# Optimization experiments

Measured on AMD Instinct MI355X. Metric: run time of the kernel, lower is better.

Reference implementation:

```python
import jax, jax.numpy as jnp
import numpy as np

TEMPERATURE = 0.5
EPS = 1e-8  # torch.nn.CosineSimilarity default eps


def setup_inputs() -> dict:
    key = jax.random.key(0)
    k1, k2 = jax.random.split(key)
    B, D = 4096, 256
    z1 = jax.random.normal(k1, (B, D), dtype=jnp.float32)
    # z2 = perturbed view of z1 so positive cosine sims are positive
    # (original torch code takes log of the RAW cosine sim, which is NaN
    #  for negative positives; realistic SimCLR positives are correlated views)
    z2 = z1 + 0.1 * jax.random.normal(k2, (B, D), dtype=jnp.float32)
    return {"z1": z1, "z2": z2}


def reference(z1, z2):
    B = z1.shape[0]
    z = jnp.concatenate([z1, z2], axis=0)                      # [2B, D]
    norm = jnp.maximum(jnp.linalg.norm(z, axis=-1, keepdims=True), EPS)
    zn = z / norm
    sim = zn @ zn.T                                            # [2B, 2B] cosine sims
    # positives: sim[i, i+B] and sim[i+B, i] (RAW cosine, per original code)
    pos = jnp.concatenate([jnp.diagonal(sim, offset=B),
                           jnp.diagonal(sim, offset=-B)])      # [2B]
    # mask self-similarity diagonal to -inf before exp-sum
    diag = jnp.eye(2 * B, dtype=bool)
    sim_masked = jnp.where(diag, -jnp.inf, sim)
    denom = jnp.sum(jnp.exp(sim_masked / TEMPERATURE), axis=-1)  # [2B]
    loss = -jnp.mean(jnp.log(pos / denom))
    return loss
```

## Files before the change

kernel.cpp:

```cpp
#include <hip/hip_runtime.h>
#include <hip/hip_bf16.h>


#define NROWS 8192
#define BHALF 4096
#define DDIM  256

typedef __attribute__((ext_vector_type(4))) int   i32x4;
typedef __attribute__((ext_vector_type(8))) int   i32x8;
typedef __attribute__((ext_vector_type(4))) float f32x4;

#define SCALE1 0x7F7F7F7F
#define TWO_LOG2E 2.8853900817779268f

__device__ __forceinline__ void load_lds16(const unsigned char* g, unsigned char* l) {
    __builtin_amdgcn_global_load_lds(
        (const __attribute__((address_space(1))) void*)g,
        (__attribute__((address_space(3))) void*)l, 16, 0, 0);
}

__global__ __launch_bounds__(256) void prep_kernel(const float* __restrict__ z1,
                                                   const float* __restrict__ z2,
                                                   unsigned char* __restrict__ zn8,
                                                   float* __restrict__ posPart,
                                                   float* __restrict__ out) {
    __shared__ float sp[4];
    int wave = threadIdx.x >> 6;
    int lane = threadIdx.x & 63;
    int i    = blockIdx.x * 4 + wave;
    float4 a = reinterpret_cast<const float4*>(z1 + (size_t)i * DDIM)[lane];
    float4 b = reinterpret_cast<const float4*>(z2 + (size_t)i * DDIM)[lane];
    float ss1 = a.x * a.x + a.y * a.y + a.z * a.z + a.w * a.w;
    float ss2 = b.x * b.x + b.y * b.y + b.z * b.z + b.w * b.w;
    float dd  = a.x * b.x + a.y * b.y + a.z * b.z + a.w * b.w;
    #pragma unroll
    for (int off = 32; off; off >>= 1) {
        ss1 += __shfl_xor(ss1, off);
        ss2 += __shfl_xor(ss2, off);
        dd  += __shfl_xor(dd, off);
    }
    float n1 = fmaxf(sqrtf(ss1), 1e-8f);
    float n2 = fmaxf(sqrtf(ss2), 1e-8f);
    float i1 = 1.0f / n1, i2 = 1.0f / n2;
    int pa = __builtin_amdgcn_cvt_pk_fp8_f32(a.x * i1, a.y * i1, 0, 0);
    pa     = __builtin_amdgcn_cvt_pk_fp8_f32(a.z * i1, a.w * i1, pa, 1);
    int pb = __builtin_amdgcn_cvt_pk_fp8_f32(b.x * i2, b.y * i2, 0, 0);
    pb     = __builtin_amdgcn_cvt_pk_fp8_f32(b.z * i2, b.w * i2, pb, 1);
    reinterpret_cast<int*>(zn8 + (size_t)i * DDIM)[lane] = pa;
    reinterpret_cast<int*>(zn8 + (size_t)(i + BHALF) * DDIM)[lane] = pb;
    if (lane == 0) sp[wave] = __logf(dd * i1 * i2);
    if (blockIdx.x == 0 && threadIdx.x == 64) out[0] = 0.0f;
    __syncthreads();
    if (threadIdx.x == 0)
        posPart[blockIdx.x] = sp[0] + sp[1] + sp[2] + sp[3];
}

__global__ __launch_bounds__(256, 3) void denom_kernel(const unsigned char* __restrict__ zn8,
                                                       float* __restrict__ P) {
    __shared__ __align__(16) unsigned char sMem[32 * 1024];
    unsigned char* buf0 = sMem;
    unsigned char* buf1 = sMem + 16384;

    int x = blockIdx.x, y = blockIdx.y;
    int bi, bj;
    if (x > y) { bi = y;      bj = x - 1;  }
    else       { bi = 63 - y; bj = 63 - x; }
    int iBase = bi * 128;
    int jBase = bj * 128;
    bool isDiag = (bi == bj);

    int t    = threadIdx.x;
    int lane = t & 63;
    int wave = t >> 6;
    int col  = lane & 15;
    int quad = lane >> 4;
    int wm = wave >> 1, wn = wave & 1;

    int rowL  = t >> 4;
    int chunk = (t & 15) ^ rowL;

    {
        const unsigned char* gA = zn8 + (size_t)(iBase + rowL) * DDIM + chunk * 16;
        #pragma unroll
        for (int q = 0; q < 4; q++)
            load_lds16(gA + q * 4096, buf0 + t * 16 + q * 4096);
        #pragma unroll
        for (int q = 0; q < 4; q++)
            load_lds16(gA + 16384 + q * 4096, buf1 + t * 16 + q * 4096);
    }
    __syncthreads();

    i32x8 af[4][2];
    {
        const unsigned char* aRow = (wm ? buf1 : buf0) + (size_t)col * DDIM;
        #pragma unroll
        for (int mt = 0; mt < 4; mt++)
            #pragma unroll
            for (int ks = 0; ks < 2; ks++) {
                int g0 = ks * 8 + quad * 2;
                i32x4 lo = *(const i32x4*)(aRow + mt * 16 * DDIM + ((g0    ) ^ col) * 16);
                i32x4 hi = *(const i32x4*)(aRow + mt * 16 * DDIM + ((g0 + 1) ^ col) * 16);
                af[mt][ks] = __builtin_shufflevector(lo, hi, 0, 1, 2, 3, 4, 5, 6, 7);
            }
    }
    __syncthreads();

    {
        const unsigned char* gB = zn8 + (size_t)(jBase + rowL) * DDIM + chunk * 16;
        #pragma unroll
        for (int q = 0; q < 4; q++)
            load_lds16(gB + q * 4096, buf0 + t * 16 + q * 4096);
        #pragma unroll
        for (int q = 0; q < 4; q++)
            load_lds16(gB + 16384 + q * 4096, buf1 + t * 16 + q * 4096);
    }
    __syncthreads();

    float rs[4][4];
    #pragma unroll
    for (int mt = 0; mt < 4; mt++)
        #pragma unroll
        for (int r = 0; r < 4; r++) rs[mt][r] = 0.f;

    #pragma unroll
    for (int h = 0; h < 2; h++) {
        const unsigned char* bRow =
            (h ? buf1 : buf0) + (size_t)(wn * 32 + col) * DDIM;

        #pragma unroll
        for (int nt = 0; nt < 2; nt++) {
            i32x8 bfr[2];
            #pragma unroll
            for (int ks = 0; ks < 2; ks++) {
                int g0 = ks * 8 + quad * 2;
                i32x4 lo = *(const i32x4*)(bRow + nt * 16 * DDIM + ((g0    ) ^ col) * 16);
                i32x4 hi = *(const i32x4*)(bRow + nt * 16 * DDIM + ((g0 + 1) ^ col) * 16);
                bfr[ks] = __builtin_shufflevector(lo, hi, 0, 1, 2, 3, 4, 5, 6, 7);
            }

            float csn = 0.f;
            #pragma unroll
            for (int mt = 0; mt < 4; mt++) {
                int gi = iBase + wm * 64 + mt * 16;
                f32x4 acc = {0.f, 0.f, 0.f, 0.f};
                acc = __builtin_amdgcn_mfma_scale_f32_16x16x128_f8f6f4(
                          af[mt][0], bfr[0], acc, 0, 0, 0, SCALE1, 0, SCALE1);
                acc = __builtin_amdgcn_mfma_scale_f32_16x16x128_f8f6f4(
                          af[mt][1], bfr[1], acc, 0, 0, 0, SCALE1, 0, SCALE1);
                bool dtile = (gi == jBase + h * 64 + wn * 32 + nt * 16);
                #pragma unroll
                for (int r = 0; r < 4; r++) {
                    float e = exp2f(acc[r] * TWO_LOG2E);
                    if (dtile && (quad * 4 + r) == col) e = 0.f;
                    rs[mt][r] += e;
                    csn       += e;
                }
            }

            if (!isDiag) {
                csn += __shfl_xor(csn, 16);
                csn += __shfl_xor(csn, 32);
                if (quad == 0)
                    P[(((size_t)bj * 64 + bi) * 2 + wm) * 128
                      + h * 64 + wn * 32 + nt * 16 + col] = csn;
            }
        }
    }

    #pragma unroll
    for (int mt = 0; mt < 4; mt++)
        #pragma unroll
        for (int r = 0; r < 4; r++) {
            float v = rs[mt][r];
            v += __shfl_xor(v, 1);
            v += __shfl_xor(v, 2);
            v += __shfl_xor(v, 4);
            v += __shfl_xor(v, 8);
            rs[mt][r] = v;
        }
    if (col == 0) {
        float* Pr = P + (((size_t)bi * 64 + bj) * 2 + wn) * 128;
        #pragma unroll
        for (int mt = 0; mt < 4; mt++) {
            f32x4 v4 = { rs[mt][0], rs[mt][1], rs[mt][2], rs[mt][3] };
            *reinterpret_cast<f32x4*>(Pr + wm * 64 + mt * 16 + quad * 4) = v4;
        }
    }
}

__global__ __launch_bounds__(256) void loss_kernel(const float* __restrict__ posPart,
                                                   const float* __restrict__ P,
                                                   float* __restrict__ out) {
    __shared__ float sdata[4];
    int t = threadIdx.x;
    int i = blockIdx.x * 256 + t;
    int bi = i >> 7, r = i & 127;
    const float* p = P + ((size_t)bi << 14) + r;
    float d0 = 0.f, d1 = 0.f, d2 = 0.f, d3 = 0.f;
    #pragma unroll
    for (int k = 0; k < 128; k += 4) {
        d0 += p[(k + 0) << 7];
        d1 += p[(k + 1) << 7];
        d2 += p[(k + 2) << 7];
        d3 += p[(k + 3) << 7];
    }
    float s = __logf((d0 + d1) + (d2 + d3));
    if (t < 32) s -= 2.0f * posPart[blockIdx.x * 32 + t];
    #pragma unroll
    for (int off = 32; off; off >>= 1) s += __shfl_xor(s, off);
    if ((t & 63) == 0) sdata[t >> 6] = s;
    __syncthreads();
    if (t == 0)
        atomicAdd(out, (sdata[0] + sdata[1] + sdata[2] + sdata[3]) * (1.0f / NROWS));
}

extern "C" void kernel_launch(void* const* d_in, const int* in_sizes, int n_in,
                              void* d_out, int out_size, void* d_ws, size_t ws_size,
                              hipStream_t stream) {
    const float* z1 = (const float*)d_in[0];
    const float* z2 = (const float*)d_in[1];

    unsigned char* zn8 = (unsigned char*)d_ws;
    float* P       = (float*)((char*)d_ws + (size_t)NROWS * DDIM);
    float* posPart = P + (size_t)64 * 64 * 2 * 128;

    prep_kernel<<<BHALF / 4, 256, 0, stream>>>(z1, z2, zn8, posPart, (float*)d_out);
    denom_kernel<<<dim3(65, 32), 256, 0, stream>>>(zn8, P);
    loss_kernel<<<NROWS / 256, 256, 0, stream>>>(posPart, P, (float*)d_out);
}
```

Measured before the change: 86.65 us.

## Fuse prep, denom and loss kernels into one persistent kernel with grid barriers

```diff
diff --git a/kernel.cpp b/kernel.cpp
--- a/kernel.cpp
+++ b/kernel.cpp
@@ -5,6 +5,7 @@
 #define NROWS 8192
 #define BHALF 4096
 #define DDIM  256
+#define NBLK  768
 
 typedef __attribute__((ext_vector_type(4))) int   i32x4;
 typedef __attribute__((ext_vector_type(8))) int   i32x8;
@@ -19,199 +20,216 @@
         (__attribute__((address_space(3))) void*)l, 16, 0, 0);
 }
 
-__global__ __launch_bounds__(256) void prep_kernel(const float* __restrict__ z1,
-                                                   const float* __restrict__ z2,
-                                                   unsigned char* __restrict__ zn8,
-                                                   float* __restrict__ posPart,
-                                                   float* __restrict__ out) {
-    __shared__ float sp[4];
-    int wave = threadIdx.x >> 6;
-    int lane = threadIdx.x & 63;
-    int i    = blockIdx.x * 4 + wave;
-    float4 a = reinterpret_cast<const float4*>(z1 + (size_t)i * DDIM)[lane];
-    float4 b = reinterpret_cast<const float4*>(z2 + (size_t)i * DDIM)[lane];
-    float ss1 = a.x * a.x + a.y * a.y + a.z * a.z + a.w * a.w;
-    float ss2 = b.x * b.x + b.y * b.y + b.z * b.z + b.w * b.w;
-    float dd  = a.x * b.x + a.y * b.y + a.z * b.z + a.w * b.w;
-    #pragma unroll
-    for (int off = 32; off; off >>= 1) {
-        ss1 += __shfl_xor(ss1, off);
-        ss2 += __shfl_xor(ss2, off);
-        dd  += __shfl_xor(dd, off);
-    }
-    float n1 = fmaxf(sqrtf(ss1), 1e-8f);
-    float n2 = fmaxf(sqrtf(ss2), 1e-8f);
-    float i1 = 1.0f / n1, i2 = 1.0f / n2;
-    int pa = __builtin_amdgcn_cvt_pk_fp8_f32(a.x * i1, a.y * i1, 0, 0);
-    pa     = __builtin_amdgcn_cvt_pk_fp8_f32(a.z * i1, a.w * i1, pa, 1);
-    int pb = __builtin_amdgcn_cvt_pk_fp8_f32(b.x * i2, b.y * i2, 0, 0);
-    pb     = __builtin_amdgcn_cvt_pk_fp8_f32(b.z * i2, b.w * i2, pb, 1);
-    reinterpret_cast<int*>(zn8 + (size_t)i * DDIM)[lane] = pa;
-    reinterpret_cast<int*>(zn8 + (size_t)(i + BHALF) * DDIM)[lane] = pb;
-    if (lane == 0) sp[wave] = __logf(dd * i1 * i2);
-    if (blockIdx.x == 0 && threadIdx.x == 64) out[0] = 0.0f;
+__device__ __forceinline__ void grid_barrier(int* cnt) {
     __syncthreads();
-    if (threadIdx.x == 0)
-        posPart[blockIdx.x] = sp[0] + sp[1] + sp[2] + sp[3];
-}
-
-__global__ __launch_bounds__(256, 3) void denom_kernel(const unsigned char* __restrict__ zn8,
-                                                       float* __restrict__ P) {
+    if (threadIdx.x == 0) {
+        __threadfence();
+        atomicAdd(cnt, 1);
+        while (__hip_atomic_load(cnt, __ATOMIC_RELAXED,
+                                 __HIP_MEMORY_SCOPE_AGENT) < NBLK)
+            __builtin_amdgcn_s_sleep(2);
+        __threadfence();
+    }
+    __syncthreads();
+}
+
+__global__ __launch_bounds__(256, 3) void fused_kernel(
+        const float* __restrict__ z1, const float* __restrict__ z2,
+        unsigned char* __restrict__ zn8, float* __restrict__ posPart,
+        float* __restrict__ P, float* __restrict__ out, int* __restrict__ bar)
+{
     __shared__ __align__(16) unsigned char sMem[32 * 1024];
-    unsigned char* buf0 = sMem;
-    unsigned char* buf1 = sMem + 16384;
-
-    int x = blockIdx.x, y = blockIdx.y;
-    int bi, bj;
-    if (x > y) { bi = y;      bj = x - 1;  }
-    else       { bi = 63 - y; bj = 63 - x; }
-    int iBase = bi * 128;
-    int jBase = bj * 128;
-    bool isDiag = (bi == bj);
-
+    int bid  = blockIdx.x;
     int t    = threadIdx.x;
+    int wave = t >> 6;
     int lane = t & 63;
-    int wave = t >> 6;
-    int col  = lane & 15;
-    int quad = lane >> 4;
-    int wm = wave >> 1, wn = wave & 1;
-
-    int rowL  = t >> 4;
-    int chunk = (t & 15) ^ rowL;
 
     {
-        const unsigned char* gA = zn8 + (size_t)(iBase + rowL) * DDIM + chunk * 16;
+        float* sp = (float*)sMem;
+        for (int vb = bid; vb < 1024; vb += NBLK) {
+            int i = vb * 4 + wave;
+            float4 a = reinterpret_cast<const float4*>(z1 + (size_t)i * DDIM)[lane];
+            float4 b = reinterpret_cast<const float4*>(z2 + (size_t)i * DDIM)[lane];
+            float ss1 = a.x * a.x + a.y * a.y + a.z * a.z + a.w * a.w;
+            float ss2 = b.x * b.x + b.y * b.y + b.z * b.z + b.w * b.w;
+            float dd  = a.x * b.x + a.y * b.y + a.z * b.z + a.w * b.w;
+            #pragma unroll
+            for (int off = 32; off; off >>= 1) {
+                ss1 += __shfl_xor(ss1, off);
+                ss2 += __shfl_xor(ss2, off);
+                dd  += __shfl_xor(dd, off);
+            }
+            float n1 = fmaxf(sqrtf(ss1), 1e-8f);
+            float n2 = fmaxf(sqrtf(ss2), 1e-8f);
+            float i1 = 1.0f / n1, i2 = 1.0f / n2;
+            int pa = __builtin_amdgcn_cvt_pk_fp8_f32(a.x * i1, a.y * i1, 0, 0);
+            pa     = __builtin_amdgcn_cvt_pk_fp8_f32(a.z * i1, a.w * i1, pa, 1);
+            int pb = __builtin_amdgcn_cvt_pk_fp8_f32(b.x * i2, b.y * i2, 0, 0);
+            pb     = __builtin_amdgcn_cvt_pk_fp8_f32(b.z * i2, b.w * i2, pb, 1);
+            reinterpret_cast<int*>(zn8 + (size_t)i * DDIM)[lane] = pa;
+            reinterpret_cast<int*>(zn8 + (size_t)(i + BHALF) * DDIM)[lane] = pb;
+            if (lane == 0) sp[wave] = __logf(dd * i1 * i2);
+            __syncthreads();
+            if (t == 0) posPart[vb] = sp[0] + sp[1] + sp[2] + sp[3];
+            __syncthreads();
+        }
+        if (bid == 0 && t == 0) out[0] = 0.0f;
+    }
+    grid_barrier(bar + 0);
+
+    {
+        unsigned char* buf0 = sMem;
+        unsigned char* buf1 = sMem + 16384;
+        int col  = lane & 15;
+        int quad = lane >> 4;
+        int wm = wave >> 1, wn = wave & 1;
+        int rowL  = t >> 4;
+        int chunk = (t & 15) ^ rowL;
+
+        for (int tile = bid; tile < 2080; tile += NBLK) {
+            __syncthreads();
+
+            int x = tile % 65, y = tile / 65;
+            int bi, bj;
+            if (x > y) { bi = y;      bj = x - 1;  }
+            else       { bi = 63 - y; bj = 63 - x; }
+            int iBase = bi * 128;
+            int jBase = bj * 128;
+            bool isDiag = (bi == bj);
+
+            {
+                const unsigned char* gA = zn8 + (size_t)(iBase + rowL) * DDIM + chunk * 16;
+                #pragma unroll
+                for (int q = 0; q < 4; q++)
+                    load_lds16(gA + q * 4096, buf0 + t * 16 + q * 4096);
+                #pragma unroll
+                for (int q = 0; q < 4; q++)
+                    load_lds16(gA + 16384 + q * 4096, buf1 + t * 16 + q * 4096);
+            }
+            __syncthreads();
+
+            i32x8 af[4][2];
+            {
+                const unsigned char* aRow = (wm ? buf1 : buf0) + (size_t)col * DDIM;
+                #pragma unroll
+                for (int mt = 0; mt < 4; mt++)
+                    #pragma unroll
+                    for (int ks = 0; ks < 2; ks++) {
+                        int g0 = ks * 8 + quad * 2;
+                        i32x4 lo = *(const i32x4*)(aRow + mt * 16 * DDIM + ((g0    ) ^ col) * 16);
+                        i32x4 hi = *(const i32x4*)(aRow + mt * 16 * DDIM + ((g0 + 1) ^ col) * 16);
+                        af[mt][ks] = __builtin_shufflevector(lo, hi, 0, 1, 2, 3, 4, 5, 6, 7);
+                    }
+            }
+            __syncthreads();
+
+            {
+                const unsigned char* gB = zn8 + (size_t)(jBase + rowL) * DDIM + chunk * 16;
+                #pragma unroll
+                for (int q = 0; q < 4; q++)
+                    load_lds16(gB + q * 4096, buf0 + t * 16 + q * 4096);
+                #pragma unroll
+                for (int q = 0; q < 4; q++)
+                    load_lds16(gB + 16384 + q * 4096, buf1 + t * 16 + q * 4096);
+            }
+            __syncthreads();
+
+            float rs[4][4];
+            #pragma unroll
+            for (int mt = 0; mt < 4; mt++)
+                #pragma unroll
+                for (int r = 0; r < 4; r++) rs[mt][r] = 0.f;
+
+            #pragma unroll
+            for (int h = 0; h < 2; h++) {
+                const unsigned char* bRow =
+                    (h ? buf1 : buf0) + (size_t)(wn * 32 + col) * DDIM;
+
+                #pragma unroll
+                for (int nt = 0; nt < 2; nt++) {
+                    i32x8 bfr[2];
+                    #pragma unroll
+                    for (int ks = 0; ks < 2; ks++) {
+                        int g0 = ks * 8 + quad * 2;
+                        i32x4 lo = *(const i32x4*)(bRow + nt * 16 * DDIM + ((g0    ) ^ col) * 16);
+                        i32x4 hi = *(const i32x4*)(bRow + nt * 16 * DDIM + ((g0 + 1) ^ col) * 16);
+                        bfr[ks] = __builtin_shufflevector(lo, hi, 0, 1, 2, 3, 4, 5, 6, 7);
+                    }
+
+                    float csn = 0.f;
+                    #pragma unroll
+                    for (int mt = 0; mt < 4; mt++) {
+                        int gi = iBase + wm * 64 + mt * 16;
+                        f32x4 acc = {0.f, 0.f, 0.f, 0.f};
+                        acc = __builtin_amdgcn_mfma_scale_f32_16x16x128_f8f6f4(
+                                  af[mt][0], bfr[0], acc, 0, 0, 0, SCALE1, 0, SCALE1);
+                        acc = __builtin_amdgcn_mfma_scale_f32_16x16x128_f8f6f4(
+                                  af[mt][1], bfr[1], acc, 0, 0, 0, SCALE1, 0, SCALE1);
+                        bool dtile = (gi == jBase + h * 64 + wn * 32 + nt * 16);
+                        #pragma unroll
+                        for (int r = 0; r < 4; r++) {
+                            float e = exp2f(acc[r] * TWO_LOG2E);
+                            if (dtile && (quad * 4 + r) == col) e = 0.f;
+                            rs[mt][r] += e;
+                            csn       += e;
+                        }
+                    }
+
+                    if (!isDiag) {
+                        csn += __shfl_xor(csn, 16);
+                        csn += __shfl_xor(csn, 32);
+                        if (quad == 0)
+                            P[(((size_t)bj * 64 + bi) * 2 + wm) * 128
+                              + h * 64 + wn * 32 + nt * 16 + col] = csn;
+                    }
+                }
+            }
+
+            #pragma unroll
+            for (int mt = 0; mt < 4; mt++)
+                #pragma unroll
+                for (int r = 0; r < 4; r++) {
+                    float v = rs[mt][r];
+                    v += __shfl_xor(v, 1);
+                    v += __shfl_xor(v, 2);
+                    v += __shfl_xor(v, 4);
+                    v += __shfl_xor(v, 8);
+                    rs[mt][r] = v;
+                }
+            if (col == 0) {
+                float* Pr = P + (((size_t)bi * 64 + bj) * 2 + wn) * 128;
+                #pragma unroll
+                for (int mt = 0; mt < 4; mt++) {
+                    f32x4 v4 = { rs[mt][0], rs[mt][1], rs[mt][2], rs[mt][3] };
+                    *reinterpret_cast<f32x4*>(Pr + wm * 64 + mt * 16 + quad * 4) = v4;
+                }
+            }
+        }
+    }
+    grid_barrier(bar + 16);
+
+    if (bid < 32) {
+        float* sdata = (float*)sMem;
+        int i = bid * 256 + t;
+        int bi = i >> 7, r = i & 127;
+        const float* p = P + ((size_t)bi << 14) + r;
+        float d0 = 0.f, d1 = 0.f, d2 = 0.f, d3 = 0.f;
         #pragma unroll
-        for (int q = 0; q < 4; q++)
-            load_lds16(gA + q * 4096, buf0 + t * 16 + q * 4096);
+        for (int k = 0; k < 128; k += 4) {
+            d0 += p[(k + 0) << 7];
+            d1 += p[(k + 1) << 7];
+            d2 += p[(k + 2) << 7];
+            d3 += p[(k + 3) << 7];
+        }
+        float s = __logf((d0 + d1) + (d2 + d3));
+        if (t < 32) s -= 2.0f * posPart[bid * 32 + t];
         #pragma unroll
-        for (int q = 0; q < 4; q++)
-            load_lds16(gA + 16384 + q * 4096, buf1 + t * 16 + q * 4096);
-    }
-    __syncthreads();
-
-    i32x8 af[4][2];
-    {
-        const unsigned char* aRow = (wm ? buf1 : buf0) + (size_t)col * DDIM;
-        #pragma unroll
-        for (int mt = 0; mt < 4; mt++)
-            #pragma unroll
-            for (int ks = 0; ks < 2; ks++) {
-                int g0 = ks * 8 + quad * 2;
-                i32x4 lo = *(const i32x4*)(aRow + mt * 16 * DDIM + ((g0    ) ^ col) * 16);
-                i32x4 hi = *(const i32x4*)(aRow + mt * 16 * DDIM + ((g0 + 1) ^ col) * 16);
-                af[mt][ks] = __builtin_shufflevector(lo, hi, 0, 1, 2, 3, 4, 5, 6, 7);
-            }
-    }
-    __syncthreads();
-
-    {
-        const unsigned char* gB = zn8 + (size_t)(jBase + rowL) * DDIM + chunk * 16;
-        #pragma unroll
-        for (int q = 0; q < 4; q++)
-            load_lds16(gB + q * 4096, buf0 + t * 16 + q * 4096);
-        #pragma unroll
-        for (int q = 0; q < 4; q++)
-            load_lds16(gB + 16384 + q * 4096, buf1 + t * 16 + q * 4096);
-    }
-    __syncthreads();
-
-    float rs[4][4];
-    #pragma unroll
-    for (int mt = 0; mt < 4; mt++)
-        #pragma unroll
-        for (int r = 0; r < 4; r++) rs[mt][r] = 0.f;
-
-    #pragma unroll
-    for (int h = 0; h < 2; h++) {
-        const unsigned char* bRow =
-            (h ? buf1 : buf0) + (size_t)(wn * 32 + col) * DDIM;
-
-        #pragma unroll
-        for (int nt = 0; nt < 2; nt++) {
-            i32x8 bfr[2];
-            #pragma unroll
-            for (int ks = 0; ks < 2; ks++) {
-                int g0 = ks * 8 + quad * 2;
-                i32x4 lo = *(const i32x4*)(bRow + nt * 16 * DDIM + ((g0    ) ^ col) * 16);
-                i32x4 hi = *(const i32x4*)(bRow + nt * 16 * DDIM + ((g0 + 1) ^ col) * 16);
-                bfr[ks] = __builtin_shufflevector(lo, hi, 0, 1, 2, 3, 4, 5, 6, 7);
-            }
-
-            float csn = 0.f;
-            #pragma unroll
-            for (int mt = 0; mt < 4; mt++) {
-                int gi = iBase + wm * 64 + mt * 16;
-                f32x4 acc = {0.f, 0.f, 0.f, 0.f};
-                acc = __builtin_amdgcn_mfma_scale_f32_16x16x128_f8f6f4(
-                          af[mt][0], bfr[0], acc, 0, 0, 0, SCALE1, 0, SCALE1);
-                acc = __builtin_amdgcn_mfma_scale_f32_16x16x128_f8f6f4(
-                          af[mt][1], bfr[1], acc, 0, 0, 0, SCALE1, 0, SCALE1);
-                bool dtile = (gi == jBase + h * 64 + wn * 32 + nt * 16);
-                #pragma unroll
-                for (int r = 0; r < 4; r++) {
-                    float e = exp2f(acc[r] * TWO_LOG2E);
-                    if (dtile && (quad * 4 + r) == col) e = 0.f;
-                    rs[mt][r] += e;
-                    csn       += e;
-                }
-            }
-
-            if (!isDiag) {
-                csn += __shfl_xor(csn, 16);
-                csn += __shfl_xor(csn, 32);
-                if (quad == 0)
-                    P[(((size_t)bj * 64 + bi) * 2 + wm) * 128
-                      + h * 64 + wn * 32 + nt * 16 + col] = csn;
-            }
-        }
-    }
-
-    #pragma unroll
-    for (int mt = 0; mt < 4; mt++)
-        #pragma unroll
-        for (int r = 0; r < 4; r++) {
-            float v = rs[mt][r];
-            v += __shfl_xor(v, 1);
-            v += __shfl_xor(v, 2);
-            v += __shfl_xor(v, 4);
-            v += __shfl_xor(v, 8);
-            rs[mt][r] = v;
-        }
-    if (col == 0) {
-        float* Pr = P + (((size_t)bi * 64 + bj) * 2 + wn) * 128;
-        #pragma unroll
-        for (int mt = 0; mt < 4; mt++) {
-            f32x4 v4 = { rs[mt][0], rs[mt][1], rs[mt][2], rs[mt][3] };
-            *reinterpret_cast<f32x4*>(Pr + wm * 64 + mt * 16 + quad * 4) = v4;
-        }
-    }
-}
-
-__global__ __launch_bounds__(256) void loss_kernel(const float* __restrict__ posPart,
-                                                   const float* __restrict__ P,
-                                                   float* __restrict__ out) {
-    __shared__ float sdata[4];
-    int t = threadIdx.x;
-    int i = blockIdx.x * 256 + t;
-    int bi = i >> 7, r = i & 127;
-    const float* p = P + ((size_t)bi << 14) + r;
-    float d0 = 0.f, d1 = 0.f, d2 = 0.f, d3 = 0.f;
-    #pragma unroll
-    for (int k = 0; k < 128; k += 4) {
-        d0 += p[(k + 0) << 7];
-        d1 += p[(k + 1) << 7];
-        d2 += p[(k + 2) << 7];
-        d3 += p[(k + 3) << 7];
-    }
-    float s = __logf((d0 + d1) + (d2 + d3));
-    if (t < 32) s -= 2.0f * posPart[blockIdx.x * 32 + t];
-    #pragma unroll
-    for (int off = 32; off; off >>= 1) s += __shfl_xor(s, off);
-    if ((t & 63) == 0) sdata[t >> 6] = s;
-    __syncthreads();
-    if (t == 0)
-        atomicAdd(out, (sdata[0] + sdata[1] + sdata[2] + sdata[3]) * (1.0f / NROWS));
+        for (int off = 32; off; off >>= 1) s += __shfl_xor(s, off);
+        if ((t & 63) == 0) sdata[t >> 6] = s;
+        __syncthreads();
+        if (t == 0)
+            atomicAdd(out, (sdata[0] + sdata[1] + sdata[2] + sdata[3]) * (1.0f / NROWS));
+    }
 }
 
 extern "C" void kernel_launch(void* const* d_in, const int* in_sizes, int n_in,
@@ -219,12 +237,13 @@
                               hipStream_t stream) {
     const float* z1 = (const float*)d_in[0];
     const float* z2 = (const float*)d_in[1];
+    float* outp = (float*)d_out;
 
     unsigned char* zn8 = (unsigned char*)d_ws;
     float* P       = (float*)((char*)d_ws + (size_t)NROWS * DDIM);
     float* posPart = P + (size_t)64 * 64 * 2 * 128;
-
-    prep_kernel<<<BHALF / 4, 256, 0, stream>>>(z1, z2, zn8, posPart, (float*)d_out);
-    denom_kernel<<<dim3(65, 32), 256, 0, stream>>>(zn8, P);
-    loss_kernel<<<NROWS / 256, 256, 0, stream>>>(posPart, P, (float*)d_out);
-}
+    int*   bar     = (int*)(posPart + 1024);
+
+    hipMemsetAsync(bar, 0, 32 * sizeof(int), stream);
+    fused_kernel<<<NBLK, 256, 0, stream>>>(z1, z2, zn8, posPart, P, outp, bar);
+}
```

New measurement: 233.6 us. +169.6%, slower.
